# Performance work log

Hardware: AMD Instinct MI355X
Metric: run time of the kernel (lower is better)

## Reference

```python
import jax, jax.numpy as jnp
import numpy as np

C, INTER, RED4 = 256, 128, 64  # in_channels, inter_ch=max(C//2,32), C//4

def setup_inputs() -> dict:
    key = jax.random.key(0)
    ks = jax.random.split(key, 12)
    B, H, W = 8, 64, 64
    s = 0.02
    return {
        "x": jax.random.normal(ks[0], (B, C, H, W), dtype=jnp.float32),
        "theta_w": jax.random.normal(ks[1], (INTER, C), dtype=jnp.float32) * s,
        "phi_w": jax.random.normal(ks[2], (INTER, C), dtype=jnp.float32) * s,
        "g_w": jax.random.normal(ks[3], (INTER, C), dtype=jnp.float32) * s,
        "out_w": jax.random.normal(ks[4], (C, INTER), dtype=jnp.float32) * s,
        "bn_gamma": jnp.ones((C,), dtype=jnp.float32),
        "bn_beta": jnp.zeros((C,), dtype=jnp.float32),
        "fc1_w": jax.random.normal(ks[5], (RED4, C), dtype=jnp.float32) * s,
        "fc1_b": jnp.zeros((RED4,), dtype=jnp.float32),
        "fc2_w": jax.random.normal(ks[6], (C, RED4), dtype=jnp.float32) * s,
        "fc2_b": jnp.zeros((C,), dtype=jnp.float32),
    }

def reference(x, theta_w, phi_w, g_w, out_w, bn_gamma, bn_beta, fc1_w, fc1_b, fc2_w, fc2_b):
    B, Cc, H, W = x.shape
    N = H * W
    xf = x.reshape(B, Cc, N)                              # [B,C,N]
    # 1x1 convs == per-pixel matmuls
    theta = jnp.einsum('ic,bcn->bni', theta_w, xf)        # [B,N,I]
    phi = jnp.einsum('ic,bcn->bin', phi_w, xf)            # [B,I,N]
    g = jnp.einsum('ic,bcn->bni', g_w, xf)                # [B,N,I]
    scale = 1.0 / jnp.sqrt(jnp.asarray(theta.shape[-1], theta.dtype))
    attn = jax.nn.softmax(jnp.einsum('bni,bim->bnm', theta, phi) * scale, axis=-1)  # [B,N,N]
    out = jnp.einsum('bnm,bmi->bni', attn, g)             # [B,N,I]
    out = jnp.einsum('ci,bni->bcn', out_w, out).reshape(B, Cc, H, W)
    # BatchNorm2d (training mode: batch stats, biased variance, eps=1e-5)
    mean = out.mean(axis=(0, 2, 3))
    var = out.var(axis=(0, 2, 3))
    out = (out - mean[:, None, None]) * jax.lax.rsqrt(var[:, None, None] + 1e-5)
    out = out * bn_gamma[:, None, None] + bn_beta[:, None, None]
    # SE channel attention on the input x
    pooled = x.mean(axis=(2, 3))                          # [B,C]
    h = jax.nn.relu(pooled @ fc1_w.T + fc1_b)
    ch_w = jax.nn.sigmoid(h @ fc2_w.T + fc2_b)[:, :, None, None]
    return x + out * ch_w
```

## Files before the change

kernel.cpp:

```cpp
#include <hip/hip_runtime.h>

#define B_DIM 8
#define C_DIM 256
#define I_DIM 128
#define N_DIM 4096
#define R_DIM 64

typedef unsigned short u16;
typedef unsigned int u32;
typedef __attribute__((ext_vector_type(8))) __bf16 bf16x8;
typedef __attribute__((ext_vector_type(4))) float f32x4;
typedef __attribute__((ext_vector_type(16))) float f32x16;

union BF8 { u32 u[4]; bf16x8 v; };

__device__ __forceinline__ u16 f2bf(float f) {
    union { float f; u32 u; } v; v.f = f;
    u32 r = v.u + 0x7FFFu + ((v.u >> 16) & 1u);
    return (u16)(r >> 16);
}
__device__ __forceinline__ float bf2f(u16 h) {
    union { u32 u; float f; } v; v.u = (u32)h << 16; return v.f;
}
__device__ __forceinline__ u32 pk2(float a, float b) {
    return (u32)f2bf(a) | ((u32)f2bf(b) << 16);
}
__device__ __forceinline__ u32 pk2t(float a, float b) {
    union { float f; u32 u; } ua, ub; ua.f = a; ub.f = b;
    return __builtin_amdgcn_perm(ub.u, ua.u, 0x07060302u);
}
__device__ __forceinline__ void async16(const u16* g, u16* l) {
    __builtin_amdgcn_global_load_lds((const __attribute__((address_space(1))) void*)g,
                                     (__attribute__((address_space(3))) void*)l, 16, 0, 0);
}

#define TH_SCALE 0.1275204890136f

static constexpr size_t OFF_BNSUM = 0;
static constexpr size_t OFF_BNSQ  = 1024;
static constexpr size_t OFF_POOL  = 2048;
static constexpr size_t OFF_CHW   = 10240;
static constexpr size_t OFF_W3    = 18432;
static constexpr size_t OFF_OWB   = 215040;
static constexpr size_t OFF_AO0   = 280576;
static constexpr size_t OFF_AO1   = OFF_AO0 + 8388608;
static constexpr size_t OFF_THETA = OFF_AO1 + 8388608;
static constexpr size_t OFF_PHIT  = OFF_THETA + 8388608;
static constexpr size_t OFF_GT    = OFF_PHIT + 8388608;
static constexpr size_t OFF_L0    = OFF_GT + 8388608;
static constexpr size_t OFF_L1    = OFF_L0 + 131072;
static constexpr size_t OFF_OUT2  = OFF_L1 + 131072;

__global__ void prep_kernel(const float* __restrict__ tw, const float* __restrict__ pw,
                            const float* __restrict__ gw, const float* __restrict__ ow,
                            u16* __restrict__ w3, u16* __restrict__ owb,
                            float* __restrict__ bnzero, float* __restrict__ pooled) {
    int idx = blockIdx.x * 256 + threadIdx.x;
    if (idx < 512) bnzero[idx] = 0.f;
    if (idx < 2048) pooled[idx] = 0.f;
    if (idx < 3 * 32768) {
        const float* src = idx < 32768 ? tw : (idx < 65536 ? pw : gw);
        w3[idx] = f2bf(src[idx & 32767]);
    }
    if (idx < 32768) owb[idx] = f2bf(ow[idx]);
}

__global__ void se_kernel(const float* __restrict__ pooled,
                          const float* __restrict__ fc1w, const float* __restrict__ fc1b,
                          const float* __restrict__ fc2w, const float* __restrict__ fc2b,
                          float* __restrict__ chw) {
    int b = blockIdx.x, t = threadIdx.x;
    __shared__ float sp[C_DIM], sh[R_DIM];
    sp[t] = pooled[b * C_DIM + t] * (1.f / N_DIM);
    __syncthreads();
    if (t < R_DIM) {
        float a = fc1b[t];
        for (int c = 0; c < C_DIM; ++c) a += sp[c] * fc1w[t * C_DIM + c];
        sh[t] = a > 0.f ? a : 0.f;
    }
    __syncthreads();
    float a = fc2b[t];
    for (int j = 0; j < R_DIM; ++j) a += sh[j] * fc2w[t * R_DIM + j];
    chw[b * C_DIM + t] = 1.f / (1.f + __builtin_amdgcn_exp2f(-a * 1.44269504089f));
}

__global__ __launch_bounds__(256) void qkv_kernel(const float* __restrict__ x,
                                                  const u16* __restrict__ w3,
                                                  u16* __restrict__ theta,
                                                  u16* __restrict__ phiT,
                                                  u16* __restrict__ gT,
                                                  float* __restrict__ pooled) {
    const int bid = blockIdx.x;
    const int b = bid & 7, nt = bid >> 3;
    const int n0 = nt * 64;
    const int t = threadIdx.x, lane = t & 63, w = t >> 6;
    const int cl = lane & 31, h = lane >> 5;

    __shared__ u16 SMQ[26624];
    u16* As  = SMQ;
    u16* Ep  = SMQ;
    u16* EpG = SMQ + 17408;

    {
        const float* xb = x + ((size_t)b * C_DIM) * N_DIM + n0;
        for (int it = 0; it < 16; ++it) {
            int id = it * 256 + t;
            int c = id >> 4, l16 = id & 15;
            float4 v = *(const float4*)(xb + (size_t)c * N_DIM + l16 * 4);
            float s = (v.x + v.y) + (v.z + v.w);
            s += __shfl_xor(s, 1); s += __shfl_xor(s, 2);
            s += __shfl_xor(s, 4); s += __shfl_xor(s, 8);
            if ((t & 15) == 0) atomicAdd(&pooled[b * C_DIM + c], s);
            u32 lo = pk2t(v.x, v.y), hi = pk2t(v.z, v.w);
            u32 plo = (u32)__shfl_xor((int)lo, 16);
            u32 phi2 = (u32)__shfl_xor((int)hi, 16);
            u32 w0, w1; int nrow, cp;
            if ((c & 1) == 0) {
                w0 = __builtin_amdgcn_perm(plo, lo, 0x05040100u);
                w1 = __builtin_amdgcn_perm(plo, lo, 0x07060302u);
                nrow = 4 * l16; cp = c;
            } else {
                w0 = __builtin_amdgcn_perm(hi, phi2, 0x05040100u);
                w1 = __builtin_amdgcn_perm(hi, phi2, 0x07060302u);
                nrow = 4 * l16 + 2; cp = c - 1;
            }
            int base = (((cp >> 3) ^ (l16 & 7)) << 3) + (cp & 7);
            *(u32*)&As[nrow * 256 + base] = w0;
            *(u32*)&As[(nrow + 1) * 256 + base] = w1;
        }
    }
    __syncthreads();

    const int mt = w & 1;
    const int ip = w >> 1;
    bf16x8 afr[16];
    #pragma unroll
    for (int ks = 0; ks < 16; ++ks) {
        int r = mt * 32 + cl;
        int g = 2 * ks + h;
        afr[ks] = *(const bf16x8*)&As[r * 256 + ((g ^ ((r >> 2) & 7)) << 3)];
    }
    __syncthreads();

    f32x16 acc[6] = {};
    const u16* wz0 = w3;
    const u16* wz1 = w3 + 32768;
    const u16* wz2 = w3 + 65536;
    #pragma unroll
    for (int ks = 0; ks < 16; ++ks) {
        bf16x8 a = afr[ks];
        #pragma unroll
        for (int f = 0; f < 2; ++f) {
            size_t off = (size_t)((2 * ip + f) * 32 + cl) * C_DIM + ks * 16 + h * 8;
            acc[f]     = __builtin_amdgcn_mfma_f32_32x32x16_bf16(a, *(const bf16x8*)(wz0 + off), acc[f], 0, 0, 0);
            acc[2 + f] = __builtin_amdgcn_mfma_f32_32x32x16_bf16(a, *(const bf16x8*)(wz1 + off), acc[2 + f], 0, 0, 0);
            acc[4 + f] = __builtin_amdgcn_mfma_f32_32x32x16_bf16(a, *(const bf16x8*)(wz2 + off), acc[4 + f], 0, 0, 0);
        }
    }

    #pragma unroll
    for (int f = 0; f < 2; ++f) {
        int i = (2 * ip + f) * 32 + cl;
        #pragma unroll
        for (int r2 = 0; r2 < 4; ++r2) {
            #pragma unroll
            for (int e = 0; e < 4; ++e) {
                int n = mt * 32 + 8 * r2 + 4 * h + e;
                Ep[n * 136 + i] = f2bf(acc[f][4 * r2 + e] * TH_SCALE);
                Ep[(64 + n) * 136 + i] = f2bf(acc[2 + f][4 * r2 + e]);
            }
            u32 lo = pk2(acc[4 + f][4 * r2 + 0], acc[4 + f][4 * r2 + 1]);
            u32 hi = pk2(acc[4 + f][4 * r2 + 2], acc[4 + f][4 * r2 + 3]);
            int nb = mt * 32 + 8 * r2 + 4 * h;
            *(u32*)&EpG[i * 72 + nb] = lo;
            *(u32*)&EpG[i * 72 + nb + 2] = hi;
        }
    }
    __syncthreads();

    #pragma unroll
    for (int it = 0; it < 8; ++it) {
        int id = it * 256 + t;
        int row = id >> 4, l16 = id & 15;
        f32x4 vv = *(const f32x4*)&Ep[row * 136 + l16 * 8];
        u16* dst = (row < 64) ? theta : phiT;
        int n = row & 63;
        *(f32x4*)(dst + ((size_t)(b * N_DIM) + n0 + n) * I_DIM + l16 * 8) = vv;
    }
    #pragma unroll
    for (int it = 0; it < 4; ++it) {
        int id = it * 256 + t;
        int i = id >> 3, l8 = id & 7;
        f32x4 vv = *(const f32x4*)&EpG[i * 72 + l8 * 8];
        *(f32x4*)(gT + ((size_t)(b * I_DIM) + i) * N_DIM + n0 + l8 * 8) = vv;
    }
}

__global__ __launch_bounds__(256) void attn_kernel(const u16* __restrict__ theta,
                                                   const u16* __restrict__ phiT,
                                                   const u16* __restrict__ gT,
                                                   u16* __restrict__ ao0, u16* __restrict__ ao1,
                                                   float* __restrict__ l0, float* __restrict__ l1) {
    const int bid = blockIdx.x;
    const int b = bid & 7, mh = (bid >> 3) & 1, qt = bid >> 4;
    const int t = threadIdx.x, lane = t & 63, w = t >> 6;
    const int cl = lane & 31, h = lane >> 5;
    const int qw = qt * 128 + w * 32;

    __shared__ u16 SM[32768];

    bf16x8 qf[8];
    {
        const u16* qp = theta + ((size_t)(b * N_DIM) + qw + cl) * I_DIM + h * 8;
        #pragma unroll
        for (int ks = 0; ks < 8; ++ks) qf[ks] = *(const bf16x8*)(qp + ks * 16);
    }

    const u16* kbase = phiT + (size_t)b * N_DIM * I_DIM + (size_t)(mh * 2048) * I_DIM;
    const u16* vbase = gT + (size_t)b * I_DIM * N_DIM + mh * 2048;
    const u16* kptr[4]; const u16* vptr[4];
    #pragma unroll
    for (int it = 0; it < 4; ++it) {
        int gi = (w * 4 + it) * 64 + lane;
        int kr = gi >> 4, kg = gi & 15;
        kptr[it] = kbase + (size_t)kr * I_DIM + ((kg ^ (kr & 7)) << 3);
        int vr = gi >> 3, vg = gi & 7;
        vptr[it] = vbase + (size_t)vr * N_DIM + ((vg ^ (vr & 7)) << 3);
    }

    auto issue = [&](int p) {
        u16* Kd = SM + p * 16384;
        u16* Vd = SM + p * 16384 + 8192;
        #pragma unroll
        for (int it = 0; it < 4; ++it) { async16(kptr[it], Kd + (w * 4 + it) * 512); kptr[it] += 64 * I_DIM; }
        #pragma unroll
        for (int it = 0; it < 4; ++it) { async16(vptr[it], Vd + (w * 4 + it) * 512); vptr[it] += 64; }
    };

    float lsum = 0.f;
    f32x16 O[4] = {};

    issue(0);

    for (int mc = 0; mc < 32; ++mc) {
        const int p = mc & 1;
        __asm__ volatile("s_barrier" ::: "memory");
        if (mc < 31) {
            issue(1 - p);
            __asm__ volatile("s_waitcnt vmcnt(8)" ::: "memory");
        } else {
            __asm__ volatile("s_waitcnt vmcnt(0)" ::: "memory");
        }
        __asm__ volatile("s_barrier" ::: "memory");

        const u16* Ks = SM + p * 16384;
        const u16* Vs = SM + p * 16384 + 8192;

        u32 pk[8][2];
        #pragma unroll
        for (int mt2 = 0; mt2 < 2; ++mt2) {
            f32x16 S = {};
            #pragma unroll
            for (int ks = 0; ks < 8; ++ks) {
                int r = mt2 * 32 + cl;
                bf16x8 kf = *(const bf16x8*)&Ks[r * 128 + (((2 * ks + h) ^ (r & 7)) << 3)];
                S = __builtin_amdgcn_mfma_f32_32x32x16_bf16(kf, qf[ks], S, 0, 0, 0);
            }
            #pragma unroll
            for (int r2 = 0; r2 < 4; ++r2) {
                float p0 = __builtin_amdgcn_exp2f(S[4 * r2 + 0]);
                float p1 = __builtin_amdgcn_exp2f(S[4 * r2 + 1]);
                float p2 = __builtin_amdgcn_exp2f(S[4 * r2 + 2]);
                float p3 = __builtin_amdgcn_exp2f(S[4 * r2 + 3]);
                lsum += (p0 + p1) + (p2 + p3);
                pk[mt2 * 4 + r2][0] = pk2t(p0, p1);
                pk[mt2 * 4 + r2][1] = pk2t(p2, p3);
            }
        }

        #pragma unroll
        for (int ks = 0; ks < 4; ++ks) {
            u32 a0 = pk[2 * ks][0], a1 = pk[2 * ks][1];
            u32 b0 = pk[2 * ks + 1][0], b1 = pk[2 * ks + 1][1];
            bool hb = (h != 0);
            u32 own0 = hb ? b0 : a0, own1 = hb ? b1 : a1;
            u32 xf0 = hb ? a0 : b0, xf1 = hb ? a1 : b1;
            u32 rc0 = (u32)__shfl_xor((int)xf0, 32);
            u32 rc1 = (u32)__shfl_xor((int)xf1, 32);
            BF8 A;
            A.u[0] = hb ? rc0 : own0;
            A.u[1] = hb ? rc1 : own1;
            A.u[2] = hb ? own0 : rc0;
            A.u[3] = hb ? own1 : rc1;
            #pragma unroll
            for (int f = 0; f < 4; ++f) {
                int ir = f * 32 + cl;
                bf16x8 vf = *(const bf16x8*)&Vs[ir * 64 + (((2 * ks + h) ^ (ir & 7)) << 3)];
                O[f] = __builtin_amdgcn_mfma_f32_32x32x16_bf16(A.v, vf, O[f], 0, 0, 0);
            }
        }
    }

    lsum += __shfl_xor(lsum, 32);
    u16* aop = (mh == 0) ? ao0 : ao1;
    float* lp = (mh == 0) ? l0 : l1;
    if (h == 0) lp[(size_t)b * N_DIM + qw + cl] = lsum;

    u16* ep = SM + w * 4096;
    #pragma unroll
    for (int f = 0; f < 4; ++f)
        #pragma unroll
        for (int r2 = 0; r2 < 4; ++r2)
            #pragma unroll
            for (int e = 0; e < 4; ++e) {
                int q = 8 * r2 + 4 * h + e;
                ep[q * 128 + f * 32 + cl] = f2bf(O[f][4 * r2 + e]);
            }
    __asm__ volatile("s_waitcnt lgkmcnt(0)" ::: "memory");
    #pragma unroll
    for (int it = 0; it < 8; ++it) {
        int id = it * 64 + lane;
        int q = id >> 4, l16 = id & 15;
        f32x4 vv = *(const f32x4*)&ep[q * 128 + l16 * 8];
        *(f32x4*)(aop + ((size_t)(b * N_DIM) + qw + q) * I_DIM + l16 * 8) = vv;
    }
}

__global__ __launch_bounds__(256) void oproj_kernel(const u16* __restrict__ ao0,
                                                    const u16* __restrict__ ao1,
                                                    const float* __restrict__ l0,
                                                    const float* __restrict__ l1,
                                                    const u16* __restrict__ owb,
                                                    u16* __restrict__ out2,
                                                    float* __restrict__ bnsum,
                                                    float* __restrict__ bnsumsq) {
    const int bid = blockIdx.x;
    const int b = bid & 7, nt = bid >> 3;
    const int n0 = nt * 64;
    const int t = threadIdx.x, lane = t & 63, w = t >> 6;
    const int cl = lane & 31, h = lane >> 5;

    __shared__ u16 Ep[256 * 72];
    __shared__ float lsum[C_DIM], lsq[C_DIM];
    lsum[t] = 0.f; lsq[t] = 0.f;
    __syncthreads();

    const int mt = w & 1;
    const int nn = n0 + mt * 32 + cl;
    float inv;
    {
        float la = l0[(size_t)b * N_DIM + nn], lb = l1[(size_t)b * N_DIM + nn];
        inv = 1.f / (la + lb);
    }
    bf16x8 afr[8];
    {
        const u16* p0 = ao0 + ((size_t)(b * N_DIM) + nn) * I_DIM + h * 8;
        const u16* p1 = ao1 + ((size_t)(b * N_DIM) + nn) * I_DIM + h * 8;
        #pragma unroll
        for (int ks = 0; ks < 8; ++ks) {
            bf16x8 x0 = *(const bf16x8*)(p0 + ks * 16);
            bf16x8 x1 = *(const bf16x8*)(p1 + ks * 16);
            const u16* u0 = (const u16*)&x0;
            const u16* u1 = (const u16*)&x1;
            float c0 = (bf2f(u0[0]) + bf2f(u1[0])) * inv;
            float c1 = (bf2f(u0[1]) + bf2f(u1[1])) * inv;
            float c2 = (bf2f(u0[2]) + bf2f(u1[2])) * inv;
            float c3 = (bf2f(u0[3]) + bf2f(u1[3])) * inv;
            float c4 = (bf2f(u0[4]) + bf2f(u1[4])) * inv;
            float c5 = (bf2f(u0[5]) + bf2f(u1[5])) * inv;
            float c6 = (bf2f(u0[6]) + bf2f(u1[6])) * inv;
            float c7 = (bf2f(u0[7]) + bf2f(u1[7])) * inv;
            BF8 r;
            r.u[0] = pk2(c0, c1); r.u[1] = pk2(c2, c3);
            r.u[2] = pk2(c4, c5); r.u[3] = pk2(c6, c7);
            afr[ks] = r.v;
        }
    }

    f32x16 D[4] = {};
    #pragma unroll
    for (int ks = 0; ks < 8; ++ks) {
        #pragma unroll
        for (int j = 0; j < 4; ++j) {
            int cr = ((w >> 1) * 4 + j) * 32 + cl;
            bf16x8 bfr = *(const bf16x8*)(owb + (size_t)cr * I_DIM + ks * 16 + h * 8);
            D[j] = __builtin_amdgcn_mfma_f32_32x32x16_bf16(afr[ks], bfr, D[j], 0, 0, 0);
        }
    }

    #pragma unroll
    for (int j = 0; j < 4; ++j) {
        int c = ((w >> 1) * 4 + j) * 32 + cl;
        float s1 = 0.f, s2 = 0.f;
        #pragma unroll
        for (int r2 = 0; r2 < 4; ++r2) {
            float v0 = D[j][4 * r2 + 0], v1 = D[j][4 * r2 + 1];
            float v2 = D[j][4 * r2 + 2], v3 = D[j][4 * r2 + 3];
            s1 += (v0 + v1) + (v2 + v3);
            s2 += (v0 * v0 + v1 * v1) + (v2 * v2 + v3 * v3);
            int nb = mt * 32 + 8 * r2 + 4 * h;
            *(u32*)&Ep[c * 72 + nb] = pk2(v0, v1);
            *(u32*)&Ep[c * 72 + nb + 2] = pk2(v2, v3);
        }
        atomicAdd(&lsum[c], s1);
        atomicAdd(&lsq[c], s2);
    }
    __syncthreads();
    #pragma unroll
    for (int it = 0; it < 8; ++it) {
        int id = it * 256 + t;
        int c = id >> 3, l8 = id & 7;
        f32x4 vv = *(const f32x4*)&Ep[c * 72 + l8 * 8];
        *(f32x4*)(out2 + ((size_t)(b * C_DIM) + c) * N_DIM + n0 + l8 * 8) = vv;
    }
    atomicAdd(&bnsum[t], lsum[t]);
    atomicAdd(&bnsumsq[t], lsq[t]);
}

__global__ void final_kernel(const float* __restrict__ x, const u16* __restrict__ out2,
                             const float* __restrict__ bnsum, const float* __restrict__ bnsumsq,
                             const float* __restrict__ gamma, const float* __restrict__ beta,
                             const float* __restrict__ chw, float* __restrict__ out) {
    int idx = blockIdx.x * 256 + threadIdx.x;
    int e = idx * 4;
    int b = e >> 20;
    int c = (e >> 12) & 255;
    float mean = bnsum[c] * (1.f / 32768.f);
    float var = bnsumsq[c] * (1.f / 32768.f) - mean * mean;
    float sc = gamma[c] * rsqrtf(var + 1e-5f);
    float sh = beta[c] - mean * sc;
    float cw = chw[b * C_DIM + c];
    ushort4 o16 = ((const ushort4*)out2)[idx];
    float4 xv = ((const float4*)x)[idx];
    float4 res;
    res.x = xv.x + (bf2f(o16.x) * sc + sh) * cw;
    res.y = xv.y + (bf2f(o16.y) * sc + sh) * cw;
    res.z = xv.z + (bf2f(o16.z) * sc + sh) * cw;
    res.w = xv.w + (bf2f(o16.w) * sc + sh) * cw;
    ((float4*)out)[idx] = res;
}

extern "C" void kernel_launch(void* const* d_in, const int* in_sizes, int n_in,
                              void* d_out, int out_size, void* d_ws, size_t ws_size,
                              hipStream_t stream) {
    const float* x   = (const float*)d_in[0];
    const float* tw  = (const float*)d_in[1];
    const float* pw  = (const float*)d_in[2];
    const float* gw  = (const float*)d_in[3];
    const float* ow  = (const float*)d_in[4];
    const float* gam = (const float*)d_in[5];
    const float* bet = (const float*)d_in[6];
    const float* f1w = (const float*)d_in[7];
    const float* f1b = (const float*)d_in[8];
    const float* f2w = (const float*)d_in[9];
    const float* f2b = (const float*)d_in[10];
    float* out = (float*)d_out;

    char* ws = (char*)d_ws;
    float* bnsum   = (float*)(ws + OFF_BNSUM);
    float* bnsumsq = (float*)(ws + OFF_BNSQ);
    float* pooled  = (float*)(ws + OFF_POOL);
    float* chw     = (float*)(ws + OFF_CHW);
    u16*   w3      = (u16*)(ws + OFF_W3);
    u16*   owb     = (u16*)(ws + OFF_OWB);
    u16*   ao0     = (u16*)(ws + OFF_AO0);
    u16*   ao1     = (u16*)(ws + OFF_AO1);
    u16*   theta   = (u16*)(ws + OFF_THETA);
    u16*   phiT    = (u16*)(ws + OFF_PHIT);
    u16*   gT      = (u16*)(ws + OFF_GT);
    float* l0      = (float*)(ws + OFF_L0);
    float* l1      = (float*)(ws + OFF_L1);
    u16*   out2    = (u16*)(ws + OFF_OUT2);

    prep_kernel<<<384, 256, 0, stream>>>(tw, pw, gw, ow, w3, owb, bnsum, pooled);
    qkv_kernel<<<512, 256, 0, stream>>>(x, w3, theta, phiT, gT, pooled);
    se_kernel<<<B_DIM, 256, 0, stream>>>(pooled, f1w, f1b, f2w, f2b, chw);
    attn_kernel<<<512, 256, 0, stream>>>(theta, phiT, gT, ao0, ao1, l0, l1);
    oproj_kernel<<<512, 256, 0, stream>>>(ao0, ao1, l0, l1, owb, out2, bnsum, bnsumsq);
    final_kernel<<<8192, 256, 0, stream>>>(x, out2, bnsum, bnsumsq, gam, bet, chw, out);
}
```

Before: 275.2 us.

## Parallelize SE MLP, split QK accumulation chains, defer softmax normalization in oproj

The SE kernel's first FC layer now runs across all 256 threads with vectorized float4 loads and a shared-memory reduction, and the second layer uses vectorized loads. In attention, the QK^T MFMA accumulation is split into two independent chains that are summed afterwards, which shortens the dependency chain. In the output projection, the two partial attention outputs are fed directly as MFMA A-operands instead of being converted, summed and rescaled first, and the 1/l normalization is applied to the accumulator afterwards from shared memory. The projection therefore issues twice as many MFMAs in exchange for dropping the per-element unpack and repack work.

Result: no change. 277.4 us (+0.8%).

```diff
diff --git a/kernel.cpp b/kernel.cpp
--- a/kernel.cpp
+++ b/kernel.cpp
@@ -65,23 +65,43 @@
     if (idx < 32768) owb[idx] = f2bf(ow[idx]);
 }
 
-__global__ void se_kernel(const float* __restrict__ pooled,
+__global__ __launch_bounds__(256) void se_kernel(const float* __restrict__ pooled,
                           const float* __restrict__ fc1w, const float* __restrict__ fc1b,
                           const float* __restrict__ fc2w, const float* __restrict__ fc2b,
                           float* __restrict__ chw) {
     int b = blockIdx.x, t = threadIdx.x;
-    __shared__ float sp[C_DIM], sh[R_DIM];
+    __shared__ float sp[C_DIM], red[C_DIM], sh[R_DIM];
     sp[t] = pooled[b * C_DIM + t] * (1.f / N_DIM);
     __syncthreads();
+    {
+        int hh = t & 63, ck = t >> 6;
+        const float4* w4 = (const float4*)(fc1w + hh * C_DIM + ck * 64);
+        const float4* s4 = (const float4*)&sp[ck * 64];
+        float a = 0.f;
+        #pragma unroll
+        for (int i = 0; i < 16; ++i) {
+            float4 wv = w4[i], xv = s4[i];
+            a += wv.x * xv.x + wv.y * xv.y + wv.z * xv.z + wv.w * xv.w;
+        }
+        red[t] = a;
+    }
+    __syncthreads();
     if (t < R_DIM) {
-        float a = fc1b[t];
-        for (int c = 0; c < C_DIM; ++c) a += sp[c] * fc1w[t * C_DIM + c];
+        float a = red[t] + red[64 + t] + red[128 + t] + red[192 + t] + fc1b[t];
         sh[t] = a > 0.f ? a : 0.f;
     }
     __syncthreads();
-    float a = fc2b[t];
-    for (int j = 0; j < R_DIM; ++j) a += sh[j] * fc2w[t * R_DIM + j];
-    chw[b * C_DIM + t] = 1.f / (1.f + __builtin_amdgcn_exp2f(-a * 1.44269504089f));
+    {
+        const float4* w4 = (const float4*)(fc2w + t * R_DIM);
+        const float4* s4 = (const float4*)sh;
+        float a = fc2b[t];
+        #pragma unroll
+        for (int i = 0; i < 16; ++i) {
+            float4 wv = w4[i], xv = s4[i];
+            a += wv.x * xv.x + wv.y * xv.y + wv.z * xv.z + wv.w * xv.w;
+        }
+        chw[b * C_DIM + t] = 1.f / (1.f + __builtin_amdgcn_exp2f(-a * 1.44269504089f));
+    }
 }
 
 __global__ __launch_bounds__(256) void qkv_kernel(const float* __restrict__ x,
@@ -259,13 +279,20 @@
         u32 pk[8][2];
         #pragma unroll
         for (int mt2 = 0; mt2 < 2; ++mt2) {
-            f32x16 S = {};
-            #pragma unroll
-            for (int ks = 0; ks < 8; ++ks) {
+            f32x16 Sa = {}, Sb = {};
+            #pragma unroll
+            for (int ks = 0; ks < 4; ++ks) {
                 int r = mt2 * 32 + cl;
                 bf16x8 kf = *(const bf16x8*)&Ks[r * 128 + (((2 * ks + h) ^ (r & 7)) << 3)];
-                S = __builtin_amdgcn_mfma_f32_32x32x16_bf16(kf, qf[ks], S, 0, 0, 0);
-            }
+                Sa = __builtin_amdgcn_mfma_f32_32x32x16_bf16(kf, qf[ks], Sa, 0, 0, 0);
+            }
+            #pragma unroll
+            for (int ks = 4; ks < 8; ++ks) {
+                int r = mt2 * 32 + cl;
+                bf16x8 kf = *(const bf16x8*)&Ks[r * 128 + (((2 * ks + h) ^ (r & 7)) << 3)];
+                Sb = __builtin_amdgcn_mfma_f32_32x32x16_bf16(kf, qf[ks], Sb, 0, 0, 0);
+            }
+            f32x16 S = Sa + Sb;
             #pragma unroll
             for (int r2 = 0; r2 < 4; ++r2) {
                 float p0 = __builtin_amdgcn_exp2f(S[4 * r2 + 0]);
@@ -341,52 +368,36 @@
     const int cl = lane & 31, h = lane >> 5;
 
     __shared__ u16 Ep[256 * 72];
-    __shared__ float lsum[C_DIM], lsq[C_DIM];
+    __shared__ float lsum[C_DIM], lsq[C_DIM], linvS[64];
     lsum[t] = 0.f; lsq[t] = 0.f;
+    if (t < 64) {
+        size_t ix = (size_t)b * N_DIM + n0 + t;
+        linvS[t] = 1.f / (l0[ix] + l1[ix]);
+    }
     __syncthreads();
 
     const int mt = w & 1;
     const int nn = n0 + mt * 32 + cl;
-    float inv;
-    {
-        float la = l0[(size_t)b * N_DIM + nn], lb = l1[(size_t)b * N_DIM + nn];
-        inv = 1.f / (la + lb);
-    }
-    bf16x8 afr[8];
-    {
-        const u16* p0 = ao0 + ((size_t)(b * N_DIM) + nn) * I_DIM + h * 8;
-        const u16* p1 = ao1 + ((size_t)(b * N_DIM) + nn) * I_DIM + h * 8;
-        #pragma unroll
-        for (int ks = 0; ks < 8; ++ks) {
-            bf16x8 x0 = *(const bf16x8*)(p0 + ks * 16);
-            bf16x8 x1 = *(const bf16x8*)(p1 + ks * 16);
-            const u16* u0 = (const u16*)&x0;
-            const u16* u1 = (const u16*)&x1;
-            float c0 = (bf2f(u0[0]) + bf2f(u1[0])) * inv;
-            float c1 = (bf2f(u0[1]) + bf2f(u1[1])) * inv;
-            float c2 = (bf2f(u0[2]) + bf2f(u1[2])) * inv;
-            float c3 = (bf2f(u0[3]) + bf2f(u1[3])) * inv;
-            float c4 = (bf2f(u0[4]) + bf2f(u1[4])) * inv;
-            float c5 = (bf2f(u0[5]) + bf2f(u1[5])) * inv;
-            float c6 = (bf2f(u0[6]) + bf2f(u1[6])) * inv;
-            float c7 = (bf2f(u0[7]) + bf2f(u1[7])) * inv;
-            BF8 r;
-            r.u[0] = pk2(c0, c1); r.u[1] = pk2(c2, c3);
-            r.u[2] = pk2(c4, c5); r.u[3] = pk2(c6, c7);
-            afr[ks] = r.v;
-        }
-    }
+    const u16* p0 = ao0 + ((size_t)(b * N_DIM) + nn) * I_DIM + h * 8;
+    const u16* p1 = ao1 + ((size_t)(b * N_DIM) + nn) * I_DIM + h * 8;
 
     f32x16 D[4] = {};
     #pragma unroll
     for (int ks = 0; ks < 8; ++ks) {
+        bf16x8 a0 = *(const bf16x8*)(p0 + ks * 16);
+        bf16x8 a1 = *(const bf16x8*)(p1 + ks * 16);
         #pragma unroll
         for (int j = 0; j < 4; ++j) {
             int cr = ((w >> 1) * 4 + j) * 32 + cl;
             bf16x8 bfr = *(const bf16x8*)(owb + (size_t)cr * I_DIM + ks * 16 + h * 8);
-            D[j] = __builtin_amdgcn_mfma_f32_32x32x16_bf16(afr[ks], bfr, D[j], 0, 0, 0);
-        }
-    }
+            D[j] = __builtin_amdgcn_mfma_f32_32x32x16_bf16(a0, bfr, D[j], 0, 0, 0);
+            D[j] = __builtin_amdgcn_mfma_f32_32x32x16_bf16(a1, bfr, D[j], 0, 0, 0);
+        }
+    }
+
+    f32x4 lv[4];
+    #pragma unroll
+    for (int r2 = 0; r2 < 4; ++r2) lv[r2] = *(const f32x4*)&linvS[mt * 32 + 8 * r2 + 4 * h];
 
     #pragma unroll
     for (int j = 0; j < 4; ++j) {
@@ -394,8 +405,8 @@
         float s1 = 0.f, s2 = 0.f;
         #pragma unroll
         for (int r2 = 0; r2 < 4; ++r2) {
-            float v0 = D[j][4 * r2 + 0], v1 = D[j][4 * r2 + 1];
-            float v2 = D[j][4 * r2 + 2], v3 = D[j][4 * r2 + 3];
+            float v0 = D[j][4 * r2 + 0] * lv[r2][0], v1 = D[j][4 * r2 + 1] * lv[r2][1];
+            float v2 = D[j][4 * r2 + 2] * lv[r2][2], v3 = D[j][4 * r2 + 3] * lv[r2][3];
             s1 += (v0 + v1) + (v2 + v3);
             s2 += (v0 * v0 + v1 * v1) + (v2 * v2 + v3 * v3);
             int nb = mt * 32 + 8 * r2 + 4 * h;
```
